# Kernel optimization log

Measured on AMD Instinct MI355X. Metric: run time of the kernel, lower is better.

## Reference

```python
import jax, jax.numpy as jnp
import numpy as np

N_NODES = 50000
N_EDGES = 800000
N_GRAPHS = 64
F_IN = 128
HEADS = 4
CH = 32
HID = HEADS * CH  # 128
N_CLASSES = 10
N_LAYERS = 3
NEG_SLOPE = 0.2


def setup_inputs() -> dict:
    key = jax.random.key(0)
    ks = jax.random.split(key, 12)
    x = jax.random.normal(ks[0], (N_NODES, F_IN), dtype=jnp.float32)
    edge_index = jax.random.randint(ks[1], (2, N_EDGES), 0, N_NODES, dtype=jnp.int64)
    batch = jnp.sort(jax.random.randint(ks[2], (N_NODES,), 0, N_GRAPHS, dtype=jnp.int64))
    s = 0.1
    Wl = jax.random.normal(ks[3], (N_LAYERS, F_IN, HID), dtype=jnp.float32) * s
    Wr = jax.random.normal(ks[4], (N_LAYERS, F_IN, HID), dtype=jnp.float32) * s
    bl = jax.random.normal(ks[5], (N_LAYERS, HID), dtype=jnp.float32) * s
    br = jax.random.normal(ks[6], (N_LAYERS, HID), dtype=jnp.float32) * s
    att = jax.random.normal(ks[7], (N_LAYERS, HEADS, CH), dtype=jnp.float32) * s
    bias = jax.random.normal(ks[8], (N_LAYERS, HID), dtype=jnp.float32) * s
    lin_w = jax.random.normal(ks[9], (HID, N_CLASSES), dtype=jnp.float32) * s
    lin_b = jax.random.normal(ks[10], (N_CLASSES,), dtype=jnp.float32) * s
    return {"x": x, "edge_index": edge_index, "batch": batch, "Wl": Wl, "Wr": Wr,
            "bl": bl, "br": br, "att": att, "bias": bias, "lin_w": lin_w, "lin_b": lin_b}


def gatv2_layer(x, Wl, Wr, bl, br, att, bias, src, dst):
    # x: [N, D_in] -> out: [N, HEADS*CH]
    n = x.shape[0]
    xl = (x @ Wl + bl).reshape(n, HEADS, CH)  # source transform
    xr = (x @ Wr + br).reshape(n, HEADS, CH)  # target transform
    # GATv2 edge scores: a^T LeakyReLU(W_l x_j + W_r x_i), per head
    e = jnp.einsum('ehc,hc->eh', jax.nn.leaky_relu(xl[src] + xr[dst], NEG_SLOPE), att)  # [E, H]
    # softmax over edges sharing the same destination node
    m = jax.ops.segment_max(e, dst, num_segments=n)
    ee = jnp.exp(e - m[dst])
    denom = jax.ops.segment_sum(ee, dst, num_segments=n)
    alpha = ee / denom[dst]  # [E, H]
    out = jax.ops.segment_sum(xl[src] * alpha[:, :, None], dst, num_segments=n)  # [N, H, C]
    return out.reshape(n, HID) + bias


def reference(x, edge_index, batch, Wl, Wr, bl, br, att, bias, lin_w, lin_b):
    n = x.shape[0]
    loop = jnp.arange(n, dtype=edge_index.dtype)
    src = jnp.concatenate([edge_index[0], loop])  # self loops (PyG default)
    dst = jnp.concatenate([edge_index[1], loop])
    h = x
    for l in range(N_LAYERS):
        h = jax.nn.elu(gatv2_layer(h, Wl[l], Wr[l], bl[l], br[l], att[l], bias[l], src, dst))
    # global mean pool over graphs
    sums = jax.ops.segment_sum(h, batch, num_segments=N_GRAPHS)
    cnt = jax.ops.segment_sum(jnp.ones((n,), h.dtype), batch, num_segments=N_GRAPHS)
    pooled = sums / jnp.maximum(cnt, 1.0)[:, None]
    logits = jax.nn.elu(pooled @ lin_w + lin_b)
    return jax.nn.log_softmax(logits, axis=1)
```

## Files before the change

### kernel.cpp

```cpp
#include <hip/hip_runtime.h>
#include <hip/hip_bf16.h>
#include <math.h>

#define N_NODES 50000
#define N_EDGES 800000
#define N_GRAPHS 64
#define HID 128
#define N_CLASSES 10
#define N_LAYERS 3
#define NEG_SLOPE 0.2f

#define NB 196
#define BCAP 5120
#define ACHUNK 4096

typedef __attribute__((ext_vector_type(8))) short short8;
typedef __attribute__((ext_vector_type(4))) float f32x4;

__device__ inline ushort f2bf(float f) {
    uint u = __builtin_bit_cast(uint, f);
    u += 0x7fffu + ((u >> 16) & 1u);
    return (ushort)(u >> 16);
}
__device__ inline float bflo(uint v) { return __builtin_bit_cast(float, v << 16); }
__device__ inline float bfhi(uint v) { return __builtin_bit_cast(float, v & 0xffff0000u); }


__global__ void prep_kernel(const float* __restrict__ x, uint* __restrict__ xb, int xtot,
                            const float* __restrict__ Wl, const float* __restrict__ Wr,
                            uint* __restrict__ wt, int wtot) {
    int i = blockIdx.x * blockDim.x + threadIdx.x;
    if (i < xtot) {
        float2 v = ((const float2*)x)[i];
        xb[i] = (uint)f2bf(v.x) | ((uint)f2bf(v.y) << 16);
        return;
    }
    i -= xtot;
    if (i >= wtot) return;
    int kp = i & 63;
    int nn = (i >> 6) & 255;
    int l  = i >> 14;
    const float* W = (nn < 128) ? Wl : Wr;
    int c = nn & 127;
    float a = W[l * 16384 + (2 * kp) * 128 + c];
    float b = W[l * 16384 + (2 * kp + 1) * 128 + c];
    wt[i] = (uint)f2bf(a) | ((uint)f2bf(b) << 16);
}


__global__ __launch_bounds__(256) void partition_kernel(
    const int* __restrict__ ei, int E, int n,
    int* __restrict__ bptr, uint* __restrict__ bbuf) {
    __shared__ int hcnt[NB];
    __shared__ int hexcl[NB];
    __shared__ int lofs[NB];
    __shared__ int delta[NB];
    __shared__ int stmp[256];
    __shared__ uint stage[ACHUNK];
    __shared__ ushort sbk[ACHUNK];
    int t = threadIdx.x;
    int total = E + n;
    int base = blockIdx.x * ACHUNK;
    int cntblk = min(ACHUNK, total - base);
    if (t < NB) { hcnt[t] = 0; lofs[t] = 0; }
    __syncthreads();

    uint v[16]; ushort bk[16];
#pragma unroll
    for (int j = 0; j < 16; ++j) {
        int e = base + j * 256 + t;
        bk[j] = 0xffff;
        if (e < total) {
            int s, d;
            if (e < E) { s = ei[e]; d = ei[E + e]; }
            else       { s = e - E; d = e - E; }
            uint b = (uint)d >> 8;
            v[j] = ((uint)s << 8) | ((uint)d & 255u);
            bk[j] = (ushort)b;
            atomicAdd(&hcnt[b], 1);
        }
    }
    __syncthreads();
    int hv = (t < NB) ? hcnt[t] : 0;
    stmp[t] = hv;
    __syncthreads();
    for (int off = 1; off < 256; off <<= 1) {
        int u = (t >= off) ? stmp[t - off] : 0;
        __syncthreads();
        stmp[t] += u;
        __syncthreads();
    }
    if (t < NB) hexcl[t] = stmp[t] - hv;
    __syncthreads();
#pragma unroll
    for (int j = 0; j < 16; ++j) {
        if (bk[j] != 0xffff) {
            int b = bk[j];
            int pos = hexcl[b] + atomicAdd(&lofs[b], 1);
            stage[pos] = v[j];
            sbk[pos] = (ushort)b;
        }
    }
    __syncthreads();
    if (t < NB) {
        int c = hcnt[t];
        int gb = c ? atomicAdd(&bptr[t], c) : 0;
        delta[t] = t * BCAP + gb - hexcl[t];
    }
    __syncthreads();
    for (int idx = t; idx < cntblk; idx += 256) {
        int b = sbk[idx];
        int tgt = delta[b] + idx;
        if (tgt < (b + 1) * BCAP) bbuf[tgt] = stage[idx];
    }
}

__global__ __launch_bounds__(256) void bscan_kernel(const int* __restrict__ bptr,
                                                    int* __restrict__ bstart,
                                                    int* __restrict__ row_start, int n) {
    __shared__ int s[256];
    int t = threadIdx.x;
    int v = (t < NB) ? min(bptr[t], BCAP) : 0;
    s[t] = v;
    __syncthreads();
    for (int off = 1; off < 256; off <<= 1) {
        int u = (t >= off) ? s[t - off] : 0;
        __syncthreads();
        s[t] += u;
        __syncthreads();
    }
    if (t < NB) bstart[t] = s[t] - v;
    if (t == NB) { bstart[NB] = s[NB - 1]; row_start[n] = s[NB - 1]; }
}

__global__ __launch_bounds__(256) void bucket_csr_kernel(
    const int* __restrict__ bptr, const int* __restrict__ bstart,
    const uint* __restrict__ bbuf, int n,
    int* __restrict__ row_start, int* __restrict__ ssrc) {
    int b = blockIdx.x;
    int t = threadIdx.x;
    int cnt = min(bptr[b], BCAP);
    int base = bstart[b];
    __shared__ int h[256], hx[256], lofs[256];
    h[t] = 0; lofs[t] = 0;
    __syncthreads();
    const uint* bp = bbuf + (size_t)b * BCAP;
    for (int k = t; k < cnt; k += 256) atomicAdd(&h[bp[k] & 255u], 1);
    __syncthreads();
    int hv = h[t];
    hx[t] = hv;
    __syncthreads();
    for (int off = 1; off < 256; off <<= 1) {
        int u = (t >= off) ? hx[t - off] : 0;
        __syncthreads();
        hx[t] += u;
        __syncthreads();
    }
    int excl = hx[t] - hv;
    int node = (b << 8) + t;
    if (node < n) row_start[node] = base + excl;
    __syncthreads();
    h[t] = excl;
    __syncthreads();
    for (int k = t; k < cnt; k += 256) {
        uint val = bp[k];
        int dl = val & 255u;
        int pos = base + h[dl] + atomicAdd(&lofs[dl], 1);
        ssrc[pos] = (int)(val & 0xffffff00u);
    }
}


__global__ __launch_bounds__(256) void gemm_mfma(
    const ushort* __restrict__ A,
    const ushort* __restrict__ Wt,
    const float* __restrict__ bl, const float* __restrict__ br,
    ushort* __restrict__ xlb, ushort* __restrict__ xrb, int n) {
    int wv = threadIdx.x >> 6;
    int lane = threadIdx.x & 63;
    int q = lane >> 4, m16 = lane & 15;
    int m0 = blockIdx.x * 64;

    short8 bf[4][4];
#pragma unroll
    for (int nt = 0; nt < 4; ++nt) {
        const ushort* wp = Wt + (size_t)(wv * 64 + nt * 16 + m16) * 128 + q * 8;
#pragma unroll
        for (int ks = 0; ks < 4; ++ks) bf[nt][ks] = *(const short8*)(wp + ks * 32);
    }
    const ushort* ap[4];
#pragma unroll
    for (int mt = 0; mt < 4; ++mt) {
        int r = m0 + mt * 16 + m16;
        if (r > n - 1) r = n - 1;
        ap[mt] = A + (size_t)r * 128 + q * 8;
    }

    f32x4 z = {0.f, 0.f, 0.f, 0.f};
    f32x4 acc[4][4];
#pragma unroll
    for (int mt = 0; mt < 4; ++mt)
#pragma unroll
        for (int nt = 0; nt < 4; ++nt) acc[mt][nt] = z;

#pragma unroll
    for (int ks = 0; ks < 4; ++ks) {
        short8 af[4];
#pragma unroll
        for (int mt = 0; mt < 4; ++mt) af[mt] = *(const short8*)(ap[mt] + ks * 32);
#pragma unroll
        for (int mt = 0; mt < 4; ++mt)
#pragma unroll
            for (int nt = 0; nt < 4; ++nt)
                acc[mt][nt] = __builtin_amdgcn_mfma_f32_16x16x32_bf16(
                    bf[nt][ks], af[mt], acc[mt][nt], 0, 0, 0);
    }

    ushort* outp = (wv >= 2) ? xrb : xlb;
    const float* bx = (wv >= 2) ? br : bl;
    int fb = (wv & 1) * 64;
#pragma unroll
    for (int nt = 0; nt < 4; ++nt) {
        int fcol = fb + nt * 16 + q * 4;
        float4 b4 = *(const float4*)&bx[fcol];
#pragma unroll
        for (int mt = 0; mt < 4; ++mt) {
            int m = m0 + mt * 16 + m16;
            if (m < n) {
                ushort4 pk;
                pk.x = f2bf(acc[mt][nt][0] + b4.x);
                pk.y = f2bf(acc[mt][nt][1] + b4.y);
                pk.z = f2bf(acc[mt][nt][2] + b4.z);
                pk.w = f2bf(acc[mt][nt][3] + b4.w);
                *(ushort4*)&outp[(size_t)m * 128 + fcol] = pk;
            }
        }
    }
}


__global__ __launch_bounds__(256) void attn_kernel(
    const uint* __restrict__ xlb, const uint* __restrict__ xrb,
    const float* __restrict__ att, const float* __restrict__ bias,
    const int* __restrict__ row_start, const int* __restrict__ ssrc,
    uint* __restrict__ hout, int n) {
    int wave = threadIdx.x >> 6;
    int lane = threadIdx.x & 63;
    int half = lane >> 5;
    int l32  = lane & 31;
    int i = blockIdx.x * 4 + wave;
    if (i >= n) return;

    const char* xlB = (const char*)xlb;
    int lofs = l32 * 8;

    uint2 xru = *(const uint2*)((const char*)xrb + (size_t)i * 256 + lofs);
    float xr0 = bflo(xru.x), xr1 = bfhi(xru.x), xr2 = bflo(xru.y), xr3 = bfhi(xru.y);
    const float L2E = 1.4426950408889634f;
    float4 at = ((const float4*)att)[l32];
    float atx = at.x * L2E, aty = at.y * L2E, atz = at.z * L2E, atw = at.w * L2E;

    int p0 = row_start[i], p1 = row_start[i + 1];

    float den0 = 0.f, den1 = 0.f;
    float b00 = 0.f, b01 = 0.f, b02 = 0.f, b03 = 0.f;
    float b10 = 0.f, b11 = 0.f, b12 = 0.f, b13 = 0.f;

    int p = p0;
    for (; p + 4 <= p1; p += 4) {
        uint s0 = (uint)ssrc[p + half];
        uint s1 = (uint)ssrc[p + 2 + half];
        uint2 u0 = *(const uint2*)(xlB + (size_t)s0 + lofs);
        uint2 u1 = *(const uint2*)(xlB + (size_t)s1 + lofs);
        float c00 = bflo(u0.x), c01 = bfhi(u0.x), c02 = bflo(u0.y), c03 = bfhi(u0.y);
        float c10 = bflo(u1.x), c11 = bfhi(u1.x), c12 = bflo(u1.y), c13 = bfhi(u1.y);
        float t, e0, e1;
        t = c00 + xr0; t = fmaxf(t, 0.2f * t); e0  = atx * t;
        t = c01 + xr1; t = fmaxf(t, 0.2f * t); e0 += aty * t;
        t = c02 + xr2; t = fmaxf(t, 0.2f * t); e0 += atz * t;
        t = c03 + xr3; t = fmaxf(t, 0.2f * t); e0 += atw * t;
        t = c10 + xr0; t = fmaxf(t, 0.2f * t); e1  = atx * t;
        t = c11 + xr1; t = fmaxf(t, 0.2f * t); e1 += aty * t;
        t = c12 + xr2; t = fmaxf(t, 0.2f * t); e1 += atz * t;
        t = c13 + xr3; t = fmaxf(t, 0.2f * t); e1 += atw * t;
        e0 += __shfl_xor(e0, 1);  e1 += __shfl_xor(e1, 1);
        e0 += __shfl_xor(e0, 2);  e1 += __shfl_xor(e1, 2);
        e0 += __shfl_xor(e0, 4);  e1 += __shfl_xor(e1, 4);
        float w0 = exp2f(e0), w1 = exp2f(e1);
        den0 += w0; den1 += w1;
        b00 += w0 * c00; b01 += w0 * c01; b02 += w0 * c02; b03 += w0 * c03;
        b10 += w1 * c10; b11 += w1 * c11; b12 += w1 * c12; b13 += w1 * c13;
    }
    if (p < p1) {
        int eA = p + half, eB = p + 2 + half;
        int lst = p1 - 1;
        uint s0 = (uint)ssrc[min(eA, lst)];
        uint s1 = (uint)ssrc[min(eB, lst)];
        uint2 u0 = *(const uint2*)(xlB + (size_t)s0 + lofs);
        uint2 u1 = *(const uint2*)(xlB + (size_t)s1 + lofs);
        float c00 = bflo(u0.x), c01 = bfhi(u0.x), c02 = bflo(u0.y), c03 = bfhi(u0.y);
        float c10 = bflo(u1.x), c11 = bfhi(u1.x), c12 = bflo(u1.y), c13 = bfhi(u1.y);
        float t, e0, e1;
        t = c00 + xr0; t = fmaxf(t, 0.2f * t); e0  = atx * t;
        t = c01 + xr1; t = fmaxf(t, 0.2f * t); e0 += aty * t;
        t = c02 + xr2; t = fmaxf(t, 0.2f * t); e0 += atz * t;
        t = c03 + xr3; t = fmaxf(t, 0.2f * t); e0 += atw * t;
        t = c10 + xr0; t = fmaxf(t, 0.2f * t); e1  = atx * t;
        t = c11 + xr1; t = fmaxf(t, 0.2f * t); e1 += aty * t;
        t = c12 + xr2; t = fmaxf(t, 0.2f * t); e1 += atz * t;
        t = c13 + xr3; t = fmaxf(t, 0.2f * t); e1 += atw * t;
        e0 += __shfl_xor(e0, 1);  e1 += __shfl_xor(e1, 1);
        e0 += __shfl_xor(e0, 2);  e1 += __shfl_xor(e1, 2);
        e0 += __shfl_xor(e0, 4);  e1 += __shfl_xor(e1, 4);
        float w0 = (eA < p1) ? exp2f(e0) : 0.f;
        float w1 = (eB < p1) ? exp2f(e1) : 0.f;
        den0 += w0; den1 += w1;
        b00 += w0 * c00; b01 += w0 * c01; b02 += w0 * c02; b03 += w0 * c03;
        b10 += w1 * c10; b11 += w1 * c11; b12 += w1 * c12; b13 += w1 * c13;
    }

    float den = den0 + den1;
    float a0 = b00 + b10, a1 = b01 + b11, a2 = b02 + b12, a3 = b03 + b13;
    den += __shfl_xor(den, 32);
    a0 += __shfl_xor(a0, 32);
    a1 += __shfl_xor(a1, 32);
    a2 += __shfl_xor(a2, 32);
    a3 += __shfl_xor(a3, 32);

    if (half == 0) {
        float inv = 1.f / den;
        float4 bi = ((const float4*)bias)[l32];
        float o0 = a0 * inv + bi.x; o0 = o0 > 0.f ? o0 : __expf(o0) - 1.f;
        float o1 = a1 * inv + bi.y; o1 = o1 > 0.f ? o1 : __expf(o1) - 1.f;
        float o2 = a2 * inv + bi.z; o2 = o2 > 0.f ? o2 : __expf(o2) - 1.f;
        float o3 = a3 * inv + bi.w; o3 = o3 > 0.f ? o3 : __expf(o3) - 1.f;
        uint2 pk;
        pk.x = (uint)f2bf(o0) | ((uint)f2bf(o1) << 16);
        pk.y = (uint)f2bf(o2) | ((uint)f2bf(o3) << 16);
        *(uint2*)((char*)hout + (size_t)i * 256 + lofs) = pk;
    }
}


__global__ __launch_bounds__(256) void pool_kernel(const uint* __restrict__ h2,
                                                   const int* __restrict__ batch, int n,
                                                   float* __restrict__ psum) {
    int g = blockIdx.x;
    int t = threadIdx.x;
    int cp = t & 63;
    int sub = (t >> 6) | (blockIdx.y << 2);
    int b, e;
    {
        int lo = 0, hi = n;
        while (lo < hi) { int mid = (lo + hi) >> 1; if (batch[mid] < g) lo = mid + 1; else hi = mid; }
        b = lo;
        lo = 0; hi = n;
        int g1 = g + 1;
        while (lo < hi) { int mid = (lo + hi) >> 1; if (batch[mid] < g1) lo = mid + 1; else hi = mid; }
        e = lo;
    }
    float a0 = 0.f, a1 = 0.f;
    for (int i = b + sub; i < e; i += 32) {
        uint u = h2[(size_t)i * 64 + cp];
        a0 += bflo(u); a1 += bfhi(u);
    }
    __shared__ float r0[256], r1[256];
    r0[t] = a0; r1[t] = a1;
    __syncthreads();
    if (t < 64) {
        float s0 = r0[t] + r0[t + 64] + r0[t + 128] + r0[t + 192];
        float s1 = r1[t] + r1[t + 64] + r1[t + 128] + r1[t + 192];
        atomicAdd(&psum[g * 128 + 2 * t], s0);
        atomicAdd(&psum[g * 128 + 2 * t + 1], s1);
    }
}

__global__ void final_kernel(const float* __restrict__ psum, const int* __restrict__ batch,
                             int n, const float* __restrict__ lw,
                             const float* __restrict__ lb, float* __restrict__ out) {
    int g = threadIdx.x;
    if (g >= N_GRAPHS) return;
    int b, e;
    {
        int lo = 0, hi = n;
        while (lo < hi) { int mid = (lo + hi) >> 1; if (batch[mid] < g) lo = mid + 1; else hi = mid; }
        b = lo;
        lo = 0; hi = n;
        int g1 = g + 1;
        while (lo < hi) { int mid = (lo + hi) >> 1; if (batch[mid] < g1) lo = mid + 1; else hi = mid; }
        e = lo;
    }
    float invc = 1.f / fmaxf((float)(e - b), 1.f);
    float z[N_CLASSES];
#pragma unroll
    for (int c = 0; c < N_CLASSES; ++c) z[c] = lb[c];
    for (int k = 0; k < 128; ++k) {
        float p = psum[g * 128 + k] * invc;
#pragma unroll
        for (int c = 0; c < N_CLASSES; ++c) z[c] += p * lw[k * N_CLASSES + c];
    }
    float mx = -1e30f;
#pragma unroll
    for (int c = 0; c < N_CLASSES; ++c) {
        z[c] = z[c] > 0.f ? z[c] : expf(z[c]) - 1.f;
        mx = fmaxf(mx, z[c]);
    }
    float s = 0.f;
#pragma unroll
    for (int c = 0; c < N_CLASSES; ++c) s += expf(z[c] - mx);
    float lse = mx + logf(s);
#pragma unroll
    for (int c = 0; c < N_CLASSES; ++c) out[g * N_CLASSES + c] = z[c] - lse;
}


extern "C" void kernel_launch(void* const* d_in, const int* in_sizes, int n_in,
                              void* d_out, int out_size, void* d_ws, size_t ws_size,
                              hipStream_t stream) {
    const float* x     = (const float*)d_in[0];
    const int*   ei    = (const int*)d_in[1];
    const int*   batch = (const int*)d_in[2];
    const float* Wl    = (const float*)d_in[3];
    const float* Wr    = (const float*)d_in[4];
    const float* bl    = (const float*)d_in[5];
    const float* br    = (const float*)d_in[6];
    const float* att   = (const float*)d_in[7];
    const float* bias  = (const float*)d_in[8];
    const float* lw    = (const float*)d_in[9];
    const float* lb    = (const float*)d_in[10];
    float* out = (float*)d_out;

    const int n = in_sizes[2];
    const int E = in_sizes[1] / 2;
    const int total_edges = E + n;

    char* ws = (char*)d_ws;
    size_t o = 0;
    auto alloc = [&](size_t bytes) -> void* {
        void* p = ws + o;
        o = (o + bytes + 255) & ~(size_t)255;
        return p;
    };
    int*    row_start = (int*)alloc((size_t)(n + 1) * 4);
    int*    bptr      = (int*)alloc((size_t)NB * 4);
    int*    bstart    = (int*)alloc((size_t)(NB + 1) * 4);
    uint*   bbuf      = (uint*)alloc((size_t)NB * BCAP * 4);
    int*    ssrc      = (int*)alloc((size_t)total_edges * 4);
    ushort* xbf0      = (ushort*)alloc((size_t)n * HID * 2);
    ushort* xlb       = (ushort*)alloc((size_t)n * HID * 2);
    ushort* xrb       = (ushort*)alloc((size_t)n * HID * 2);
    ushort* hbA       = (ushort*)alloc((size_t)n * HID * 2);
    ushort* hbB       = (ushort*)alloc((size_t)n * HID * 2);
    uint*   wt        = (uint*)alloc((size_t)N_LAYERS * 256 * 64 * 4);
    float*  psum      = (float*)alloc((size_t)N_GRAPHS * HID * 4);

    hipMemsetAsync(bptr, 0, (size_t)NB * 4, stream);
    hipMemsetAsync(psum, 0, (size_t)N_GRAPHS * HID * 4, stream);

    int xtot = n * 64;
    int wtot = N_LAYERS * 256 * 64;
    prep_kernel<<<(xtot + wtot + 255) / 256, 256, 0, stream>>>(x, (uint*)xbf0, xtot,
                                                               Wl, Wr, wt, wtot);

    int pblocks = (total_edges + ACHUNK - 1) / ACHUNK;
    partition_kernel<<<pblocks, 256, 0, stream>>>(ei, E, n, bptr, bbuf);
    bscan_kernel<<<1, 256, 0, stream>>>(bptr, bstart, row_start, n);
    bucket_csr_kernel<<<NB, 256, 0, stream>>>(bptr, bstart, bbuf, n, row_start, ssrc);

    int mblocks = (n + 63) / 64;
    int ablocks = (n + 3) / 4;

    const ushort* hin = xbf0;
    ushort* houts[N_LAYERS] = {hbA, hbB, hbA};
    for (int l = 0; l < N_LAYERS; ++l) {
        gemm_mfma<<<mblocks, 256, 0, stream>>>(hin, (const ushort*)(wt + (size_t)l * 256 * 64),
                                               bl + l * HID, br + l * HID, xlb, xrb, n);
        attn_kernel<<<ablocks, 256, 0, stream>>>((const uint*)xlb, (const uint*)xrb,
                                                 att + l * HID, bias + l * HID,
                                                 row_start, ssrc, (uint*)houts[l], n);
        hin = houts[l];
    }

    pool_kernel<<<dim3(N_GRAPHS, 8), 256, 0, stream>>>((const uint*)hbA, batch, n, psum);
    final_kernel<<<1, 64, 0, stream>>>(psum, batch, n, lw, lb, out);
}
```

Before: 383.2 us.

## Fuse setup kernels, merge CSR build with first GEMM, fold pooling into last attention

Several kernels are merged. Bf16 conversion of x and W and the edge partition now run in one setup kernel. The bucket scan and per-bucket CSR build are folded into the layer-0 GEMM launch as extra blocks. The last attention layer atomically accumulates its output into the per-graph pool sums, so the pool kernel and the write-back of h are gone. The attention edge loop is unrolled to 8 edges per iteration, and the packed edge encoding changes to 16-bit src/dst fields. This cuts launch count and one pass over the hidden state, at the cost of many float atomics on 64x128 pool sums and heavier per-thread code.

```diff
diff --git a/kernel.cpp b/kernel.cpp
--- a/kernel.cpp
+++ b/kernel.cpp
@@ -22,67 +22,79 @@
     u += 0x7fffu + ((u >> 16) & 1u);
     return (ushort)(u >> 16);
 }
+__device__ inline uint pk2bf(float a, float b) {
+    return (uint)f2bf(a) | ((uint)f2bf(b) << 16);
+}
 __device__ inline float bflo(uint v) { return __builtin_bit_cast(float, v << 16); }
 __device__ inline float bfhi(uint v) { return __builtin_bit_cast(float, v & 0xffff0000u); }
 
 
-__global__ void prep_kernel(const float* __restrict__ x, uint* __restrict__ xb, int xtot,
-                            const float* __restrict__ Wl, const float* __restrict__ Wr,
-                            uint* __restrict__ wt, int wtot) {
-    int i = blockIdx.x * blockDim.x + threadIdx.x;
-    if (i < xtot) {
-        float2 v = ((const float2*)x)[i];
-        xb[i] = (uint)f2bf(v.x) | ((uint)f2bf(v.y) << 16);
+__global__ __launch_bounds__(256) void setup_kernel(
+    const float* __restrict__ x, uint* __restrict__ xb, int n,
+    const float* __restrict__ Wl, const float* __restrict__ Wr,
+    uint* __restrict__ wt, int wtot,
+    const int* __restrict__ ei, int E,
+    int* __restrict__ bptr, uint* __restrict__ bbuf,
+    int xqb, int wb) {
+    __shared__ int hcnt[256];
+    __shared__ int hexcl[256];
+    __shared__ int lofs[256];
+    __shared__ int delta[256];
+    __shared__ uint stage[ACHUNK];
+    int t = threadIdx.x;
+    int blk = blockIdx.x;
+
+    if (blk < xqb) {
+        int j = blk * 256 + t;
+        if (j < n * 16) {
+            const float4* xp = (const float4*)x + (size_t)j * 2;
+            float4 a = xp[0], b = xp[1];
+            uint4 o;
+            o.x = pk2bf(a.x, a.y); o.y = pk2bf(a.z, a.w);
+            o.z = pk2bf(b.x, b.y); o.w = pk2bf(b.z, b.w);
+            ((uint4*)xb)[j] = o;
+        }
         return;
     }
-    i -= xtot;
-    if (i >= wtot) return;
-    int kp = i & 63;
-    int nn = (i >> 6) & 255;
-    int l  = i >> 14;
-    const float* W = (nn < 128) ? Wl : Wr;
-    int c = nn & 127;
-    float a = W[l * 16384 + (2 * kp) * 128 + c];
-    float b = W[l * 16384 + (2 * kp + 1) * 128 + c];
-    wt[i] = (uint)f2bf(a) | ((uint)f2bf(b) << 16);
-}
-
-
-__global__ __launch_bounds__(256) void partition_kernel(
-    const int* __restrict__ ei, int E, int n,
-    int* __restrict__ bptr, uint* __restrict__ bbuf) {
-    __shared__ int hcnt[NB];
-    __shared__ int hexcl[NB];
-    __shared__ int lofs[NB];
-    __shared__ int delta[NB];
-    __shared__ int stmp[256];
-    __shared__ uint stage[ACHUNK];
-    __shared__ ushort sbk[ACHUNK];
-    int t = threadIdx.x;
+    blk -= xqb;
+    if (blk < wb) {
+        int i = blk * 256 + t;
+        if (i >= wtot) return;
+        int kp = i & 63;
+        int nn = (i >> 6) & 255;
+        int l  = i >> 14;
+        const float* W = (nn < 128) ? Wl : Wr;
+        int c = nn & 127;
+        wt[i] = pk2bf(W[l * 16384 + (2 * kp) * 128 + c],
+                      W[l * 16384 + (2 * kp + 1) * 128 + c]);
+        return;
+    }
+    blk -= wb;
     int total = E + n;
-    int base = blockIdx.x * ACHUNK;
+    int base = blk * ACHUNK;
     int cntblk = min(ACHUNK, total - base);
-    if (t < NB) { hcnt[t] = 0; lofs[t] = 0; }
-    __syncthreads();
-
-    uint v[16]; ushort bk[16];
+    hcnt[t] = 0; lofs[t] = 0;
+    __syncthreads();
+
+    uint v[16]; int bk[16];
 #pragma unroll
     for (int j = 0; j < 16; ++j) {
         int e = base + j * 256 + t;
-        bk[j] = 0xffff;
+        bk[j] = -1;
         if (e < total) {
             int s, d;
             if (e < E) { s = ei[e]; d = ei[E + e]; }
             else       { s = e - E; d = e - E; }
-            uint b = (uint)d >> 8;
-            v[j] = ((uint)s << 8) | ((uint)d & 255u);
-            bk[j] = (ushort)b;
-            atomicAdd(&hcnt[b], 1);
+            v[j] = ((uint)s << 16) | (uint)d;
+            bk[j] = d >> 8;
+            atomicAdd(&hcnt[bk[j]], 1);
         }
     }
     __syncthreads();
-    int hv = (t < NB) ? hcnt[t] : 0;
-    stmp[t] = hv;
+    int hv = hcnt[t];
+    int sc = hv;
+    __shared__ int stmp[256];
+    stmp[t] = sc;
     __syncthreads();
     for (int off = 1; off < 256; off <<= 1) {
         int u = (t >= off) ? stmp[t - off] : 0;
@@ -90,15 +102,13 @@
         stmp[t] += u;
         __syncthreads();
     }
-    if (t < NB) hexcl[t] = stmp[t] - hv;
+    hexcl[t] = stmp[t] - hv;
     __syncthreads();
 #pragma unroll
     for (int j = 0; j < 16; ++j) {
-        if (bk[j] != 0xffff) {
-            int b = bk[j];
-            int pos = hexcl[b] + atomicAdd(&lofs[b], 1);
+        if (bk[j] >= 0) {
+            int pos = hexcl[bk[j]] + atomicAdd(&lofs[bk[j]], 1);
             stage[pos] = v[j];
-            sbk[pos] = (ushort)b;
         }
     }
     __syncthreads();
@@ -109,77 +119,22 @@
     }
     __syncthreads();
     for (int idx = t; idx < cntblk; idx += 256) {
-        int b = sbk[idx];
+        uint val = stage[idx];
+        int b = (val >> 8) & 0xff;
         int tgt = delta[b] + idx;
-        if (tgt < (b + 1) * BCAP) bbuf[tgt] = stage[idx];
-    }
-}
-
-__global__ __launch_bounds__(256) void bscan_kernel(const int* __restrict__ bptr,
-                                                    int* __restrict__ bstart,
-                                                    int* __restrict__ row_start, int n) {
-    __shared__ int s[256];
-    int t = threadIdx.x;
-    int v = (t < NB) ? min(bptr[t], BCAP) : 0;
-    s[t] = v;
-    __syncthreads();
-    for (int off = 1; off < 256; off <<= 1) {
-        int u = (t >= off) ? s[t - off] : 0;
-        __syncthreads();
-        s[t] += u;
-        __syncthreads();
-    }
-    if (t < NB) bstart[t] = s[t] - v;
-    if (t == NB) { bstart[NB] = s[NB - 1]; row_start[n] = s[NB - 1]; }
-}
-
-__global__ __launch_bounds__(256) void bucket_csr_kernel(
-    const int* __restrict__ bptr, const int* __restrict__ bstart,
-    const uint* __restrict__ bbuf, int n,
-    int* __restrict__ row_start, int* __restrict__ ssrc) {
-    int b = blockIdx.x;
-    int t = threadIdx.x;
-    int cnt = min(bptr[b], BCAP);
-    int base = bstart[b];
-    __shared__ int h[256], hx[256], lofs[256];
-    h[t] = 0; lofs[t] = 0;
-    __syncthreads();
-    const uint* bp = bbuf + (size_t)b * BCAP;
-    for (int k = t; k < cnt; k += 256) atomicAdd(&h[bp[k] & 255u], 1);
-    __syncthreads();
-    int hv = h[t];
-    hx[t] = hv;
-    __syncthreads();
-    for (int off = 1; off < 256; off <<= 1) {
-        int u = (t >= off) ? hx[t - off] : 0;
-        __syncthreads();
-        hx[t] += u;
-        __syncthreads();
-    }
-    int excl = hx[t] - hv;
-    int node = (b << 8) + t;
-    if (node < n) row_start[node] = base + excl;
-    __syncthreads();
-    h[t] = excl;
-    __syncthreads();
-    for (int k = t; k < cnt; k += 256) {
-        uint val = bp[k];
-        int dl = val & 255u;
-        int pos = base + h[dl] + atomicAdd(&lofs[dl], 1);
-        ssrc[pos] = (int)(val & 0xffffff00u);
-    }
-}
-
-
-__global__ __launch_bounds__(256) void gemm_mfma(
-    const ushort* __restrict__ A,
-    const ushort* __restrict__ Wt,
+        if (tgt < (b + 1) * BCAP) bbuf[tgt] = val;
+    }
+}
+
+
+__device__ __forceinline__ void gemm_body(
+    const ushort* __restrict__ A, const ushort* __restrict__ Wt,
     const float* __restrict__ bl, const float* __restrict__ br,
-    ushort* __restrict__ xlb, ushort* __restrict__ xrb, int n) {
-    int wv = threadIdx.x >> 6;
-    int lane = threadIdx.x & 63;
+    ushort* __restrict__ xlb, ushort* __restrict__ xrb, int n, int bid, int tid) {
+    int wv = tid >> 6;
+    int lane = tid & 63;
     int q = lane >> 4, m16 = lane & 15;
-    int m0 = blockIdx.x * 64;
+    int m0 = bid * 64;
 
     short8 bf[4][4];
 #pragma unroll
@@ -238,12 +193,83 @@
     }
 }
 
+__global__ __launch_bounds__(256) void csr_gemm0_kernel(
+    const int* __restrict__ bptr, const uint* __restrict__ bbuf, int n,
+    int* __restrict__ row_start, int* __restrict__ ssrc,
+    const ushort* __restrict__ A, const ushort* __restrict__ Wt,
+    const float* __restrict__ bl, const float* __restrict__ br,
+    ushort* __restrict__ xlb, ushort* __restrict__ xrb) {
+    int t = threadIdx.x;
+    if (blockIdx.x >= NB) {
+        gemm_body(A, Wt, bl, br, xlb, xrb, n, blockIdx.x - NB, t);
+        return;
+    }
+    int b = blockIdx.x;
+    __shared__ int sb[256], h[256], hx[256], lofs[256];
+    int bv = (t < NB) ? min(bptr[t], BCAP) : 0;
+    sb[t] = bv;
+    __syncthreads();
+    for (int off = 1; off < 256; off <<= 1) {
+        int u = (t >= off) ? sb[t - off] : 0;
+        __syncthreads();
+        sb[t] += u;
+        __syncthreads();
+    }
+    int cnt = min(bptr[b], BCAP);
+    int base = sb[b] - cnt;
+    if (b == NB - 1 && t == 0) row_start[n] = sb[NB - 1];
+    h[t] = 0; lofs[t] = 0;
+    __syncthreads();
+    const uint* bp = bbuf + (size_t)b * BCAP;
+    for (int k = t; k < cnt; k += 256) atomicAdd(&h[bp[k] & 255u], 1);
+    __syncthreads();
+    int hv = h[t];
+    hx[t] = hv;
+    __syncthreads();
+    for (int off = 1; off < 256; off <<= 1) {
+        int u = (t >= off) ? hx[t - off] : 0;
+        __syncthreads();
+        hx[t] += u;
+        __syncthreads();
+    }
+    int excl = hx[t] - hv;
+    int node = (b << 8) + t;
+    if (node < n) row_start[node] = base + excl;
+    __syncthreads();
+    h[t] = excl;
+    __syncthreads();
+    for (int k = t; k < cnt; k += 256) {
+        uint val = bp[k];
+        int dl = val & 255u;
+        int pos = base + h[dl] + atomicAdd(&lofs[dl], 1);
+        ssrc[pos] = (int)((val & 0xffff0000u) >> 8);
+    }
+}
+
+__global__ __launch_bounds__(256) void gemm_mfma(
+    const ushort* __restrict__ A, const ushort* __restrict__ Wt,
+    const float* __restrict__ bl, const float* __restrict__ br,
+    ushort* __restrict__ xlb, ushort* __restrict__ xrb, int n) {
+    gemm_body(A, Wt, bl, br, xlb, xrb, n, blockIdx.x, threadIdx.x);
+}
+
+
+#define EDGE_MATH(u, c0, c1, c2, c3, e)                                  \
+    {                                                                    \
+        float t_;                                                        \
+        c0 = bflo(u.x); c1 = bfhi(u.x); c2 = bflo(u.y); c3 = bfhi(u.y);  \
+        t_ = c0 + xr0; t_ = fmaxf(t_, 0.2f * t_); e  = atx * t_;         \
+        t_ = c1 + xr1; t_ = fmaxf(t_, 0.2f * t_); e += aty * t_;         \
+        t_ = c2 + xr2; t_ = fmaxf(t_, 0.2f * t_); e += atz * t_;         \
+        t_ = c3 + xr3; t_ = fmaxf(t_, 0.2f * t_); e += atw * t_;         \
+    }
 
 __global__ __launch_bounds__(256) void attn_kernel(
     const uint* __restrict__ xlb, const uint* __restrict__ xrb,
     const float* __restrict__ att, const float* __restrict__ bias,
     const int* __restrict__ row_start, const int* __restrict__ ssrc,
-    uint* __restrict__ hout, int n) {
+    uint* __restrict__ hout, float* __restrict__ psum,
+    const int* __restrict__ batch, int n) {
     int wave = threadIdx.x >> 6;
     int lane = threadIdx.x & 63;
     int half = lane >> 5;
@@ -267,29 +293,52 @@
     float b10 = 0.f, b11 = 0.f, b12 = 0.f, b13 = 0.f;
 
     int p = p0;
-    for (; p + 4 <= p1; p += 4) {
+    for (; p + 8 <= p1; p += 8) {
+        uint s0 = (uint)ssrc[p + half];
+        uint s1 = (uint)ssrc[p + 2 + half];
+        uint s2 = (uint)ssrc[p + 4 + half];
+        uint s3 = (uint)ssrc[p + 6 + half];
+        uint2 u0 = *(const uint2*)(xlB + (size_t)s0 + lofs);
+        uint2 u1 = *(const uint2*)(xlB + (size_t)s1 + lofs);
+        uint2 u2 = *(const uint2*)(xlB + (size_t)s2 + lofs);
+        uint2 u3 = *(const uint2*)(xlB + (size_t)s3 + lofs);
+        float c00, c01, c02, c03, c10, c11, c12, c13;
+        float c20, c21, c22, c23, c30, c31, c32, c33;
+        float e0, e1, e2, e3;
+        EDGE_MATH(u0, c00, c01, c02, c03, e0);
+        EDGE_MATH(u1, c10, c11, c12, c13, e1);
+        EDGE_MATH(u2, c20, c21, c22, c23, e2);
+        EDGE_MATH(u3, c30, c31, c32, c33, e3);
+        e0 += __shfl_xor(e0, 1); e1 += __shfl_xor(e1, 1);
+        e2 += __shfl_xor(e2, 1); e3 += __shfl_xor(e3, 1);
+        e0 += __shfl_xor(e0, 2); e1 += __shfl_xor(e1, 2);
+        e2 += __shfl_xor(e2, 2); e3 += __shfl_xor(e3, 2);
+        e0 += __shfl_xor(e0, 4); e1 += __shfl_xor(e1, 4);
+        e2 += __shfl_xor(e2, 4); e3 += __shfl_xor(e3, 4);
+        float w0 = exp2f(e0), w1 = exp2f(e1), w2 = exp2f(e2), w3 = exp2f(e3);
+        den0 += w0 + w2; den1 += w1 + w3;
+        b00 += w0 * c00; b01 += w0 * c01; b02 += w0 * c02; b03 += w0 * c03;
+        b10 += w1 * c10; b11 += w1 * c11; b12 += w1 * c12; b13 += w1 * c13;
+        b00 += w2 * c20; b01 += w2 * c21; b02 += w2 * c22; b03 += w2 * c23;
+        b10 += w3 * c30; b11 += w3 * c31; b12 += w3 * c32; b13 += w3 * c33;
+    }
+    if (p + 4 <= p1) {
         uint s0 = (uint)ssrc[p + half];
         uint s1 = (uint)ssrc[p + 2 + half];
         uint2 u0 = *(const uint2*)(xlB + (size_t)s0 + lofs);
         uint2 u1 = *(const uint2*)(xlB + (size_t)s1 + lofs);
-        float c00 = bflo(u0.x), c01 = bfhi(u0.x), c02 = bflo(u0.y), c03 = bfhi(u0.y);
-        float c10 = bflo(u1.x), c11 = bfhi(u1.x), c12 = bflo(u1.y), c13 = bfhi(u1.y);
-        float t, e0, e1;
-        t = c00 + xr0; t = fmaxf(t, 0.2f * t); e0  = atx * t;
-        t = c01 + xr1; t = fmaxf(t, 0.2f * t); e0 += aty * t;
-        t = c02 + xr2; t = fmaxf(t, 0.2f * t); e0 += atz * t;
-        t = c03 + xr3; t = fmaxf(t, 0.2f * t); e0 += atw * t;
-        t = c10 + xr0; t = fmaxf(t, 0.2f * t); e1  = atx * t;
-        t = c11 + xr1; t = fmaxf(t, 0.2f * t); e1 += aty * t;
-        t = c12 + xr2; t = fmaxf(t, 0.2f * t); e1 += atz * t;
-        t = c13 + xr3; t = fmaxf(t, 0.2f * t); e1 += atw * t;
-        e0 += __shfl_xor(e0, 1);  e1 += __shfl_xor(e1, 1);
-        e0 += __shfl_xor(e0, 2);  e1 += __shfl_xor(e1, 2);
-        e0 += __shfl_xor(e0, 4);  e1 += __shfl_xor(e1, 4);
+        float c00, c01, c02, c03, c10, c11, c12, c13;
+        float e0, e1;
+        EDGE_MATH(u0, c00, c01, c02, c03, e0);
+        EDGE_MATH(u1, c10, c11, c12, c13, e1);
+        e0 += __shfl_xor(e0, 1); e1 += __shfl_xor(e1, 1);
+        e0 += __shfl_xor(e0, 2); e1 += __shfl_xor(e1, 2);
+        e0 += __shfl_xor(e0, 4); e1 += __shfl_xor(e1, 4);
         float w0 = exp2f(e0), w1 = exp2f(e1);
         den0 += w0; den1 += w1;
         b00 += w0 * c00; b01 += w0 * c01; b02 += w0 * c02; b03 += w0 * c03;
         b10 += w1 * c10; b11 += w1 * c11; b12 += w1 * c12; b13 += w1 * c13;
+        p += 4;
     }
     if (p < p1) {
         int eA = p + half, eB = p + 2 + half;
@@ -298,20 +347,13 @@
         uint s1 = (uint)ssrc[min(eB, lst)];
         uint2 u0 = *(const uint2*)(xlB + (size_t)s0 + lofs);
         uint2 u1 = *(const uint2*)(xlB + (size_t)s1 + lofs);
-        float c00 = bflo(u0.x), c01 = bfhi(u0.x), c02 = bflo(u0.y), c03 = bfhi(u0.y);
-        float c10 = bflo(u1.x), c11 = bfhi(u1.x), c12 = bflo(u1.y), c13 = bfhi(u1.y);
-        float t, e0, e1;
-        t = c00 + xr0; t = fmaxf(t, 0.2f * t); e0  = atx * t;
-        t = c01 + xr1; t = fmaxf(t, 0.2f * t); e0 += aty * t;
-        t = c02 + xr2; t = fmaxf(t, 0.2f * t); e0 += atz * t;
-        t = c03 + xr3; t = fmaxf(t, 0.2f * t); e0 += atw * t;
-        t = c10 + xr0; t = fmaxf(t, 0.2f * t); e1  = atx * t;
-        t = c11 + xr1; t = fmaxf(t, 0.2f * t); e1 += aty * t;
-        t = c12 + xr2; t = fmaxf(t, 0.2f * t); e1 += atz * t;
-        t = c13 + xr3; t = fmaxf(t, 0.2f * t); e1 += atw * t;
-        e0 += __shfl_xor(e0, 1);  e1 += __shfl_xor(e1, 1);
-        e0 += __shfl_xor(e0, 2);  e1 += __shfl_xor(e1, 2);
-        e0 += __shfl_xor(e0, 4);  e1 += __shfl_xor(e1, 4);
+        float c00, c01, c02, c03, c10, c11, c12, c13;
+        float e0, e1;
+        EDGE_MATH(u0, c00, c01, c02, c03, e0);
+        EDGE_MATH(u1, c10, c11, c12, c13, e1);
+        e0 += __shfl_xor(e0, 1); e1 += __shfl_xor(e1, 1);
+        e0 += __shfl_xor(e0, 2); e1 += __shfl_xor(e1, 2);
+        e0 += __shfl_xor(e0, 4); e1 += __shfl_xor(e1, 4);
         float w0 = (eA < p1) ? exp2f(e0) : 0.f;
         float w1 = (eB < p1) ? exp2f(e1) : 0.f;
         den0 += w0; den1 += w1;
@@ -334,46 +376,21 @@
         float o1 = a1 * inv + bi.y; o1 = o1 > 0.f ? o1 : __expf(o1) - 1.f;
         float o2 = a2 * inv + bi.z; o2 = o2 > 0.f ? o2 : __expf(o2) - 1.f;
         float o3 = a3 * inv + bi.w; o3 = o3 > 0.f ? o3 : __expf(o3) - 1.f;
-        uint2 pk;
-        pk.x = (uint)f2bf(o0) | ((uint)f2bf(o1) << 16);
-        pk.y = (uint)f2bf(o2) | ((uint)f2bf(o3) << 16);
-        *(uint2*)((char*)hout + (size_t)i * 256 + lofs) = pk;
-    }
-}
-
-
-__global__ __launch_bounds__(256) void pool_kernel(const uint* __restrict__ h2,
-                                                   const int* __restrict__ batch, int n,
-                                                   float* __restrict__ psum) {
-    int g = blockIdx.x;
-    int t = threadIdx.x;
-    int cp = t & 63;
-    int sub = (t >> 6) | (blockIdx.y << 2);
-    int b, e;
-    {
-        int lo = 0, hi = n;
-        while (lo < hi) { int mid = (lo + hi) >> 1; if (batch[mid] < g) lo = mid + 1; else hi = mid; }
-        b = lo;
-        lo = 0; hi = n;
-        int g1 = g + 1;
-        while (lo < hi) { int mid = (lo + hi) >> 1; if (batch[mid] < g1) lo = mid + 1; else hi = mid; }
-        e = lo;
-    }
-    float a0 = 0.f, a1 = 0.f;
-    for (int i = b + sub; i < e; i += 32) {
-        uint u = h2[(size_t)i * 64 + cp];
-        a0 += bflo(u); a1 += bfhi(u);
-    }
-    __shared__ float r0[256], r1[256];
-    r0[t] = a0; r1[t] = a1;
-    __syncthreads();
-    if (t < 64) {
-        float s0 = r0[t] + r0[t + 64] + r0[t + 128] + r0[t + 192];
-        float s1 = r1[t] + r1[t + 64] + r1[t + 128] + r1[t + 192];
-        atomicAdd(&psum[g * 128 + 2 * t], s0);
-        atomicAdd(&psum[g * 128 + 2 * t + 1], s1);
-    }
-}
+        if (psum) {
+            float* pp = &psum[(size_t)batch[i] * 128 + l32 * 4];
+            atomicAdd(pp + 0, o0);
+            atomicAdd(pp + 1, o1);
+            atomicAdd(pp + 2, o2);
+            atomicAdd(pp + 3, o3);
+        } else {
+            uint2 pk;
+            pk.x = pk2bf(o0, o1);
+            pk.y = pk2bf(o2, o3);
+            *(uint2*)((char*)hout + (size_t)i * 256 + lofs) = pk;
+        }
+    }
+}
+
 
 __global__ void final_kernel(const float* __restrict__ psum, const int* __restrict__ batch,
                              int n, const float* __restrict__ lw,
@@ -443,7 +460,6 @@
     };
     int*    row_start = (int*)alloc((size_t)(n + 1) * 4);
     int*    bptr      = (int*)alloc((size_t)NB * 4);
-    int*    bstart    = (int*)alloc((size_t)(NB + 1) * 4);
     uint*   bbuf      = (uint*)alloc((size_t)NB * BCAP * 4);
     int*    ssrc      = (int*)alloc((size_t)total_edges * 4);
     ushort* xbf0      = (ushort*)alloc((size_t)n * HID * 2);
@@ -457,30 +473,33 @@
     hipMemsetAsync(bptr, 0, (size_t)NB * 4, stream);
     hipMemsetAsync(psum, 0, (size_t)N_GRAPHS * HID * 4, stream);
 
-    int xtot = n * 64;
     int wtot = N_LAYERS * 256 * 64;
-    prep_kernel<<<(xtot + wtot + 255) / 256, 256, 0, stream>>>(x, (uint*)xbf0, xtot,
-                                                               Wl, Wr, wt, wtot);
-
-    int pblocks = (total_edges + ACHUNK - 1) / ACHUNK;
-    partition_kernel<<<pblocks, 256, 0, stream>>>(ei, E, n, bptr, bbuf);
-    bscan_kernel<<<1, 256, 0, stream>>>(bptr, bstart, row_start, n);
-    bucket_csr_kernel<<<NB, 256, 0, stream>>>(bptr, bstart, bbuf, n, row_start, ssrc);
+    int xqb = (n * 16 + 255) / 256;
+    int wb  = (wtot + 255) / 256;
+    int pb  = (total_edges + ACHUNK - 1) / ACHUNK;
+    setup_kernel<<<xqb + wb + pb, 256, 0, stream>>>(
+        x, (uint*)xbf0, n, Wl, Wr, wt, wtot, ei, E, bptr, bbuf, xqb, wb);
 
     int mblocks = (n + 63) / 64;
     int ablocks = (n + 3) / 4;
 
-    const ushort* hin = xbf0;
-    ushort* houts[N_LAYERS] = {hbA, hbB, hbA};
-    for (int l = 0; l < N_LAYERS; ++l) {
-        gemm_mfma<<<mblocks, 256, 0, stream>>>(hin, (const ushort*)(wt + (size_t)l * 256 * 64),
-                                               bl + l * HID, br + l * HID, xlb, xrb, n);
-        attn_kernel<<<ablocks, 256, 0, stream>>>((const uint*)xlb, (const uint*)xrb,
-                                                 att + l * HID, bias + l * HID,
-                                                 row_start, ssrc, (uint*)houts[l], n);
-        hin = houts[l];
-    }
-
-    pool_kernel<<<dim3(N_GRAPHS, 8), 256, 0, stream>>>((const uint*)hbA, batch, n, psum);
+    csr_gemm0_kernel<<<NB + mblocks, 256, 0, stream>>>(
+        bptr, bbuf, n, row_start, ssrc,
+        xbf0, (const ushort*)wt, bl, br, xlb, xrb);
+
+    attn_kernel<<<ablocks, 256, 0, stream>>>((const uint*)xlb, (const uint*)xrb,
+                                             att, bias, row_start, ssrc,
+                                             (uint*)hbA, nullptr, batch, n);
+    gemm_mfma<<<mblocks, 256, 0, stream>>>(hbA, (const ushort*)(wt + (size_t)256 * 64),
+                                           bl + HID, br + HID, xlb, xrb, n);
+    attn_kernel<<<ablocks, 256, 0, stream>>>((const uint*)xlb, (const uint*)xrb,
+                                             att + HID, bias + HID, row_start, ssrc,
+                                             (uint*)hbB, nullptr, batch, n);
+    gemm_mfma<<<mblocks, 256, 0, stream>>>(hbB, (const ushort*)(wt + (size_t)2 * 256 * 64),
+                                           bl + 2 * HID, br + 2 * HID, xlb, xrb, n);
+    attn_kernel<<<ablocks, 256, 0, stream>>>((const uint*)xlb, (const uint*)xrb,
+                                             att + 2 * HID, bias + 2 * HID, row_start, ssrc,
+                                             nullptr, psum, batch, n);
+
     final_kernel<<<1, 64, 0, stream>>>(psum, batch, n, lw, lb, out);
 }
```

New measurement: 664.8 us. 73.5% more time.
